# Kernel optimization log

Hardware: AMD Instinct MI355X
Metric: run time of the kernel (lower is better)

Reference implementation:

```python
import jax, jax.numpy as jnp
import numpy as np

EPS = 1e-5  # torch F.layer_norm default

def setup_inputs() -> dict:
    key = jax.random.key(0)
    k_h, k_v = jax.random.split(key)
    B, S, d, rank = 4, 4096, 2048, 8
    h = jax.random.normal(k_h, (B, S, d), dtype=jnp.float32)
    gamma = jnp.ones((d,), dtype=jnp.float32)
    beta = jnp.zeros((d,), dtype=jnp.float32)
    V = jax.random.normal(k_v, (rank, d), dtype=jnp.float32) * 0.01
    eta = jnp.asarray(0.1, dtype=jnp.float32)
    return {"h": h, "gamma": gamma, "beta": beta, "V": V, "eta": eta}

def reference(h, gamma, beta, V, eta):
    # LayerNorm over last dim, no affine (torch F.layer_norm with only normalized_shape)
    mu = jnp.mean(h, axis=-1, keepdims=True)
    var = jnp.mean((h - mu) ** 2, axis=-1, keepdims=True)  # biased var, matches torch
    h_hat = (h - mu) * jax.lax.rsqrt(var + EPS)
    # low-rank diffusion: h_hat @ (V^T V) == (h_hat @ V^T) @ V, O(n*d*rank)
    proj = jnp.einsum('bsr,rd->bsd', jnp.einsum('bsd,rd->bsr', h_hat, V), V)
    delta_h = h_hat - proj
    e_curv = jnp.sum(delta_h ** 2, axis=-1)  # [B, S]
    eta_c = jnp.clip(eta, 0.0, 0.5)
    h_smooth = h_hat - eta_c * delta_h
    out = h_smooth * gamma + beta
    return out, e_curv
```

## Files before the change

kernel.cpp:

```cpp
#include <hip/hip_runtime.h>
#include <hip/hip_bf16.h>


constexpr int D       = 2048;
constexpr int RANK    = 8;
constexpr int BLOCK   = 256;
constexpr int ROWS_PB = 8;
constexpr float LN_EPS = 1e-5f;

template<int CTRL, int RM>
__device__ __forceinline__ float dppadd(float x) {
    int y = __builtin_amdgcn_update_dpp(0, __float_as_int(x), CTRL, RM, 0xf, true);
    return x + __int_as_float(y);
}
__device__ __forceinline__ float dpp_sum64(float x) {
    x = dppadd<0x111, 0xf>(x);
    x = dppadd<0x112, 0xf>(x);
    x = dppadd<0x114, 0xf>(x);
    x = dppadd<0x118, 0xf>(x);
    x = dppadd<0x142, 0xa>(x);
    x = dppadd<0x143, 0xc>(x);
    return x;
}

__device__ __forceinline__ void f4acc(float4& a, const float4& b) {
    a.x += b.x; a.y += b.y; a.z += b.z; a.w += b.w;
}

__global__ __launch_bounds__(BLOCK, 2)
void lbonorm_kernel(const float* __restrict__ h,
                    const float* __restrict__ gamma,
                    const float* __restrict__ beta,
                    const float* __restrict__ V,
                    const float* __restrict__ eta_p,
                    float* __restrict__ out,
                    float* __restrict__ e_out)
{
    const int t    = threadIdx.x;
    const int lane = t & 63;
    const int wave = t >> 6;

    const int c0 = t * 4;
    const int c1 = D / 2 + t * 4;

    __shared__ __align__(16) float red[2][4][12];

    const size_t row0 = (size_t)blockIdx.x * ROWS_PB;

    float4 ha = *reinterpret_cast<const float4*>(h + row0 * (size_t)D + c0);
    float4 hb = *reinterpret_cast<const float4*>(h + row0 * (size_t)D + c1);

    float vreg[8][RANK];
    #pragma unroll
    for (int r = 0; r < RANK; ++r) {
        float4 a = *reinterpret_cast<const float4*>(V + (size_t)r * D + c0);
        float4 b = *reinterpret_cast<const float4*>(V + (size_t)r * D + c1);
        vreg[0][r] = a.x; vreg[1][r] = a.y; vreg[2][r] = a.z; vreg[3][r] = a.w;
        vreg[4][r] = b.x; vreg[5][r] = b.y; vreg[6][r] = b.z; vreg[7][r] = b.w;
    }

    const float4 g0 = *reinterpret_cast<const float4*>(gamma + c0);
    const float4 g1 = *reinterpret_cast<const float4*>(gamma + c1);
    const float4 bb0 = *reinterpret_cast<const float4*>(beta + c0);
    const float4 bb1 = *reinterpret_cast<const float4*>(beta + c1);
    const float gam[8] = {g0.x,g0.y,g0.z,g0.w,g1.x,g1.y,g1.z,g1.w};
    const float bet[8] = {bb0.x,bb0.y,bb0.z,bb0.w,bb1.x,bb1.y,bb1.z,bb1.w};
    const float eta = fminf(fmaxf(eta_p[0], 0.0f), 0.5f);

    float vsum[RANK];
    {
        float vs[RANK];
        #pragma unroll
        for (int r = 0; r < RANK; ++r) {
            float v = 0.f;
            #pragma unroll
            for (int k = 0; k < 8; ++k) v += vreg[k][r];
            vs[r] = dpp_sum64(v);
        }
        if (lane == 63) {
            float4* dst = reinterpret_cast<float4*>(&red[1][wave][0]);
            dst[0] = make_float4(vs[0], vs[1], vs[2], vs[3]);
            dst[1] = make_float4(vs[4], vs[5], vs[6], vs[7]);
        }
        __syncthreads();
        float4 qa = make_float4(0.f,0.f,0.f,0.f), qb = qa;
        #pragma unroll
        for (int w = 0; w < 4; ++w) {
            f4acc(qa, reinterpret_cast<const float4*>(&red[1][w][0])[0]);
            f4acc(qb, reinterpret_cast<const float4*>(&red[1][w][0])[1]);
        }
        vsum[0]=qa.x; vsum[1]=qa.y; vsum[2]=qa.z; vsum[3]=qa.w;
        vsum[4]=qb.x; vsum[5]=qb.y; vsum[6]=qb.z; vsum[7]=qb.w;
    }

    float ep = 0.f;

    for (int rr = 0; rr < ROWS_PB; ++rr) {
        const size_t row = row0 + rr;

        float4 na, nb;
        if (rr + 1 < ROWS_PB) {
            na = *reinterpret_cast<const float4*>(h + (row + 1) * (size_t)D + c0);
            nb = *reinterpret_cast<const float4*>(h + (row + 1) * (size_t)D + c1);
        }

        const float hr[8] = {ha.x,ha.y,ha.z,ha.w,hb.x,hb.y,hb.z,hb.w};

        float vals[11];
        {
            float s = 0.f, s2 = 0.f;
            #pragma unroll
            for (int k = 0; k < 8; ++k) { s += hr[k]; s2 = fmaf(hr[k], hr[k], s2); }
            vals[0] = s; vals[1] = s2;
            #pragma unroll
            for (int r = 0; r < RANK; ++r) {
                float dp = 0.f;
                #pragma unroll
                for (int k = 0; k < 8; ++k) dp = fmaf(hr[k], vreg[k][r], dp);
                vals[2 + r] = dp;
            }
            vals[10] = ep;
        }
        #pragma unroll
        for (int n = 0; n < 11; ++n) vals[n] = dpp_sum64(vals[n]);

        const int buf = rr & 1;
        if (lane == 63) {
            float4* dst = reinterpret_cast<float4*>(&red[buf][wave][0]);
            dst[0] = make_float4(vals[0], vals[1], vals[2], vals[3]);
            dst[1] = make_float4(vals[4], vals[5], vals[6], vals[7]);
            dst[2] = make_float4(vals[8], vals[9], vals[10], 0.f);
        }
        __syncthreads();

        float4 q0 = make_float4(0.f,0.f,0.f,0.f), q1 = q0, q2 = q0;
        #pragma unroll
        for (int w = 0; w < 4; ++w) {
            const float4* src = reinterpret_cast<const float4*>(&red[buf][w][0]);
            f4acc(q0, src[0]); f4acc(q1, src[1]); f4acc(q2, src[2]);
        }

        if (t == 0 && rr > 0) e_out[row - 1] = q2.z;

        const float mu  = q0.x * (1.0f / D);
        const float var = fmaxf(q0.y * (1.0f / D) - mu * mu, 0.0f);
        const float inv = rsqrtf(var + LN_EPS);
        const float dot[8] = {q0.z, q0.w, q1.x, q1.y, q1.z, q1.w, q2.x, q2.y};
        float c[RANK];
        #pragma unroll
        for (int r = 0; r < RANK; ++r)
            c[r] = inv * (dot[r] - mu * vsum[r]);

        float e = 0.f, ov[8];
        #pragma unroll
        for (int k = 0; k < 8; ++k) {
            const float hh = (hr[k] - mu) * inv;
            float pr = 0.f;
            #pragma unroll
            for (int r = 0; r < RANK; ++r) pr = fmaf(c[r], vreg[k][r], pr);
            const float dl = hh - pr;
            e = fmaf(dl, dl, e);
            ov[k] = fmaf(fmaf(-eta, dl, hh), gam[k], bet[k]);
        }
        ep = e;

        float* orow = out + row * (size_t)D;
        *reinterpret_cast<float4*>(orow + c0) = make_float4(ov[0], ov[1], ov[2], ov[3]);
        *reinterpret_cast<float4*>(orow + c1) = make_float4(ov[4], ov[5], ov[6], ov[7]);

        ha = na; hb = nb;
    }

    ep = dpp_sum64(ep);
    if (lane == 63) red[0][wave][0] = ep;
    __syncthreads();
    if (t == 0)
        e_out[row0 + ROWS_PB - 1] = red[0][0][0] + red[0][1][0] + red[0][2][0] + red[0][3][0];
}

extern "C" void kernel_launch(void* const* d_in, const int* in_sizes, int n_in,
                              void* d_out, int out_size, void* d_ws, size_t ws_size,
                              hipStream_t stream) {
    const float* h     = (const float*)d_in[0];
    const float* gamma = (const float*)d_in[1];
    const float* beta  = (const float*)d_in[2];
    const float* V     = (const float*)d_in[3];
    const float* eta   = (const float*)d_in[4];
    float* out = (float*)d_out;

    const int d = in_sizes[1];
    const long long rows = in_sizes[0] / d;
    float* e_out = out + (size_t)rows * d;

    dim3 grid((unsigned)(rows / ROWS_PB));
    lbonorm_kernel<<<grid, BLOCK, 0, stream>>>(h, gamma, beta, V, eta, out, e_out);
}
```

Measured before the change: 57.59 us.

## Use packed f2 FMA math, quad DPP cross-wave reduce, and two-row prefetch

Recasts the per-thread arithmetic as 2-wide float vectors so the compiler can emit packed FP32 FMA instructions (v_pk_fma_f32). The cross-wave LDS reduction changes from each thread reading all four wave partials to each lane reading one wave's slot, then combining across the quad with DPP. The h prefetch now runs two rows ahead instead of one, which hides more load latency at the cost of extra registers. Together these cut VALU and LDS instruction count in a loop that is largely memory-bound.

```diff
diff --git a/kernel.cpp b/kernel.cpp
--- a/kernel.cpp
+++ b/kernel.cpp
@@ -7,6 +7,12 @@
 constexpr int BLOCK   = 256;
 constexpr int ROWS_PB = 8;
 constexpr float LN_EPS = 1e-5f;
+
+using f2 = __attribute__((ext_vector_type(2))) float;
+
+__device__ __forceinline__ f2 f2fma(f2 a, f2 b, f2 c) {
+    return __builtin_elementwise_fma(a, b, c);
+}
 
 template<int CTRL, int RM>
 __device__ __forceinline__ float dppadd(float x) {
@@ -22,9 +28,16 @@
     x = dppadd<0x143, 0xc>(x);
     return x;
 }
-
-__device__ __forceinline__ void f4acc(float4& a, const float4& b) {
-    a.x += b.x; a.y += b.y; a.z += b.z; a.w += b.w;
+template<int PAT>
+__device__ __forceinline__ float qpadd(float x) {
+    int y = __builtin_amdgcn_update_dpp(0, __float_as_int(x), PAT, 0xf, 0xf, true);
+    return x + __int_as_float(y);
+}
+__device__ __forceinline__ void quad_reduce(float4& q) {
+    q.x = qpadd<0xB1>(q.x); q.y = qpadd<0xB1>(q.y);
+    q.z = qpadd<0xB1>(q.z); q.w = qpadd<0xB1>(q.w);
+    q.x = qpadd<0x4E>(q.x); q.y = qpadd<0x4E>(q.y);
+    q.z = qpadd<0x4E>(q.z); q.w = qpadd<0x4E>(q.w);
 }
 
 __global__ __launch_bounds__(BLOCK, 2)
@@ -49,22 +62,24 @@
 
     float4 ha = *reinterpret_cast<const float4*>(h + row0 * (size_t)D + c0);
     float4 hb = *reinterpret_cast<const float4*>(h + row0 * (size_t)D + c1);
-
-    float vreg[8][RANK];
+    float4 na = *reinterpret_cast<const float4*>(h + (row0 + 1) * (size_t)D + c0);
+    float4 nb = *reinterpret_cast<const float4*>(h + (row0 + 1) * (size_t)D + c1);
+
+    f2 vreg[4][RANK];
     #pragma unroll
     for (int r = 0; r < RANK; ++r) {
         float4 a = *reinterpret_cast<const float4*>(V + (size_t)r * D + c0);
         float4 b = *reinterpret_cast<const float4*>(V + (size_t)r * D + c1);
-        vreg[0][r] = a.x; vreg[1][r] = a.y; vreg[2][r] = a.z; vreg[3][r] = a.w;
-        vreg[4][r] = b.x; vreg[5][r] = b.y; vreg[6][r] = b.z; vreg[7][r] = b.w;
+        vreg[0][r] = f2{a.x, a.y}; vreg[1][r] = f2{a.z, a.w};
+        vreg[2][r] = f2{b.x, b.y}; vreg[3][r] = f2{b.z, b.w};
     }
 
     const float4 g0 = *reinterpret_cast<const float4*>(gamma + c0);
     const float4 g1 = *reinterpret_cast<const float4*>(gamma + c1);
     const float4 bb0 = *reinterpret_cast<const float4*>(beta + c0);
     const float4 bb1 = *reinterpret_cast<const float4*>(beta + c1);
-    const float gam[8] = {g0.x,g0.y,g0.z,g0.w,g1.x,g1.y,g1.z,g1.w};
-    const float bet[8] = {bb0.x,bb0.y,bb0.z,bb0.w,bb1.x,bb1.y,bb1.z,bb1.w};
+    const f2 gam[4] = {f2{g0.x,g0.y}, f2{g0.z,g0.w}, f2{g1.x,g1.y}, f2{g1.z,g1.w}};
+    const f2 bet[4] = {f2{bb0.x,bb0.y}, f2{bb0.z,bb0.w}, f2{bb1.x,bb1.y}, f2{bb1.z,bb1.w}};
     const float eta = fminf(fmaxf(eta_p[0], 0.0f), 0.5f);
 
     float vsum[RANK];
@@ -72,10 +87,8 @@
         float vs[RANK];
         #pragma unroll
         for (int r = 0; r < RANK; ++r) {
-            float v = 0.f;
-            #pragma unroll
-            for (int k = 0; k < 8; ++k) v += vreg[k][r];
-            vs[r] = dpp_sum64(v);
+            f2 v = vreg[0][r] + vreg[1][r] + vreg[2][r] + vreg[3][r];
+            vs[r] = dpp_sum64(v.x + v.y);
         }
         if (lane == 63) {
             float4* dst = reinterpret_cast<float4*>(&red[1][wave][0]);
@@ -83,12 +96,9 @@
             dst[1] = make_float4(vs[4], vs[5], vs[6], vs[7]);
         }
         __syncthreads();
-        float4 qa = make_float4(0.f,0.f,0.f,0.f), qb = qa;
-        #pragma unroll
-        for (int w = 0; w < 4; ++w) {
-            f4acc(qa, reinterpret_cast<const float4*>(&red[1][w][0])[0]);
-            f4acc(qb, reinterpret_cast<const float4*>(&red[1][w][0])[1]);
-        }
+        const float4* src = reinterpret_cast<const float4*>(&red[1][lane & 3][0]);
+        float4 qa = src[0], qb = src[1];
+        quad_reduce(qa); quad_reduce(qb);
         vsum[0]=qa.x; vsum[1]=qa.y; vsum[2]=qa.z; vsum[3]=qa.w;
         vsum[4]=qb.x; vsum[5]=qb.y; vsum[6]=qb.z; vsum[7]=qb.w;
     }
@@ -98,26 +108,26 @@
     for (int rr = 0; rr < ROWS_PB; ++rr) {
         const size_t row = row0 + rr;
 
-        float4 na, nb;
-        if (rr + 1 < ROWS_PB) {
-            na = *reinterpret_cast<const float4*>(h + (row + 1) * (size_t)D + c0);
-            nb = *reinterpret_cast<const float4*>(h + (row + 1) * (size_t)D + c1);
-        }
-
-        const float hr[8] = {ha.x,ha.y,ha.z,ha.w,hb.x,hb.y,hb.z,hb.w};
+        float4 pa, pb;
+        if (rr + 2 < ROWS_PB) {
+            pa = *reinterpret_cast<const float4*>(h + (row + 2) * (size_t)D + c0);
+            pb = *reinterpret_cast<const float4*>(h + (row + 2) * (size_t)D + c1);
+        }
+
+        const f2 h2[4] = {f2{ha.x,ha.y}, f2{ha.z,ha.w}, f2{hb.x,hb.y}, f2{hb.z,hb.w}};
 
         float vals[11];
         {
-            float s = 0.f, s2 = 0.f;
-            #pragma unroll
-            for (int k = 0; k < 8; ++k) { s += hr[k]; s2 = fmaf(hr[k], hr[k], s2); }
-            vals[0] = s; vals[1] = s2;
+            f2 s  = (h2[0] + h2[1]) + (h2[2] + h2[3]);
+            f2 s2 = f2fma(h2[0], h2[0], f2fma(h2[1], h2[1],
+                    f2fma(h2[2], h2[2], h2[3] * h2[3])));
+            vals[0] = s.x + s.y;
+            vals[1] = s2.x + s2.y;
             #pragma unroll
             for (int r = 0; r < RANK; ++r) {
-                float dp = 0.f;
-                #pragma unroll
-                for (int k = 0; k < 8; ++k) dp = fmaf(hr[k], vreg[k][r], dp);
-                vals[2 + r] = dp;
+                f2 d = f2fma(h2[0], vreg[0][r], f2fma(h2[1], vreg[1][r],
+                       f2fma(h2[2], vreg[2][r], h2[3] * vreg[3][r])));
+                vals[2 + r] = d.x + d.y;
             }
             vals[10] = ep;
         }
@@ -133,12 +143,9 @@
         }
         __syncthreads();
 
-        float4 q0 = make_float4(0.f,0.f,0.f,0.f), q1 = q0, q2 = q0;
-        #pragma unroll
-        for (int w = 0; w < 4; ++w) {
-            const float4* src = reinterpret_cast<const float4*>(&red[buf][w][0]);
-            f4acc(q0, src[0]); f4acc(q1, src[1]); f4acc(q2, src[2]);
-        }
+        const float4* src = reinterpret_cast<const float4*>(&red[buf][lane & 3][0]);
+        float4 q0 = src[0], q1 = src[1], q2 = src[2];
+        quad_reduce(q0); quad_reduce(q1); quad_reduce(q2);
 
         if (t == 0 && rr > 0) e_out[row - 1] = q2.z;
 
@@ -146,29 +153,38 @@
         const float var = fmaxf(q0.y * (1.0f / D) - mu * mu, 0.0f);
         const float inv = rsqrtf(var + LN_EPS);
         const float dot[8] = {q0.z, q0.w, q1.x, q1.y, q1.z, q1.w, q2.x, q2.y};
-        float c[RANK];
-        #pragma unroll
-        for (int r = 0; r < RANK; ++r)
-            c[r] = inv * (dot[r] - mu * vsum[r]);
-
-        float e = 0.f, ov[8];
-        #pragma unroll
-        for (int k = 0; k < 8; ++k) {
-            const float hh = (hr[k] - mu) * inv;
-            float pr = 0.f;
+        f2 c2[RANK];
+        #pragma unroll
+        for (int r = 0; r < RANK; ++r) {
+            const float c = inv * (dot[r] - mu * vsum[r]);
+            c2[r] = f2{c, c};
+        }
+
+        const f2 inv2  = f2{inv, inv};
+        const f2 nmi2  = f2{-mu * inv, -mu * inv};
+        const f2 neta2 = f2{-eta, -eta};
+        f2 e2 = f2{0.f, 0.f};
+        f2 ov[4];
+        #pragma unroll
+        for (int k = 0; k < 4; ++k) {
+            const f2 hh = f2fma(h2[k], inv2, nmi2);
+            f2 pr = c2[0] * vreg[0 == k ? 0 : 0][0];
+            pr = c2[0] * vreg[k][0];
             #pragma unroll
-            for (int r = 0; r < RANK; ++r) pr = fmaf(c[r], vreg[k][r], pr);
-            const float dl = hh - pr;
-            e = fmaf(dl, dl, e);
-            ov[k] = fmaf(fmaf(-eta, dl, hh), gam[k], bet[k]);
-        }
-        ep = e;
+            for (int r = 1; r < RANK; ++r) pr = f2fma(c2[r], vreg[k][r], pr);
+            const f2 dl = hh - pr;
+            e2 = f2fma(dl, dl, e2);
+            const f2 sm = f2fma(neta2, dl, hh);
+            ov[k] = f2fma(sm, gam[k], bet[k]);
+        }
+        ep = e2.x + e2.y;
 
         float* orow = out + row * (size_t)D;
-        *reinterpret_cast<float4*>(orow + c0) = make_float4(ov[0], ov[1], ov[2], ov[3]);
-        *reinterpret_cast<float4*>(orow + c1) = make_float4(ov[4], ov[5], ov[6], ov[7]);
+        *reinterpret_cast<float4*>(orow + c0) = make_float4(ov[0].x, ov[0].y, ov[1].x, ov[1].y);
+        *reinterpret_cast<float4*>(orow + c1) = make_float4(ov[2].x, ov[2].y, ov[3].x, ov[3].y);
 
         ha = na; hb = nb;
+        if (rr + 2 < ROWS_PB) { na = pa; nb = pb; }
     }
 
     ep = dpp_sum64(ep);
```

After: 56.64 us. Within noise of the previous version (-1.7%).
